# Kernel optimization log

Hardware: AMD Instinct MI355X
Metric: run time of the kernel (lower is better)

## Reference

```python
import jax, jax.numpy as jnp
import numpy as np

N_NODES = 50000
N_EDGES = 800000
D_IN, D_HID, D_OUT = 96, 96, 48


def _gcn_conv(x, src, dst, W, b, num_nodes):
    """PyG GCNConv: h = x @ W; out[dst] += norm * h[src]; out += b.
    Symmetric normalization deg^{-1/2}[src] * deg^{-1/2}[dst], self-loops included
    (src/dst already contain self-loops)."""
    h = x @ W  # [N, d_out]
    deg = jax.ops.segment_sum(jnp.ones_like(dst, dtype=h.dtype), dst,
                              num_segments=num_nodes)  # in-degree incl. self-loop
    dinv = jnp.where(deg > 0, jax.lax.rsqrt(deg), 0.0)
    norm = dinv[src] * dinv[dst]  # [E+N]
    msgs = h[src] * norm[:, None]  # gather + scale (the memory-bound part)
    out = jax.ops.segment_sum(msgs, dst, num_segments=num_nodes)  # scatter-add
    return out + b


def setup_inputs() -> dict:
    key = jax.random.key(0)
    k1, k2, k3, k4 = jax.random.split(key, 4)
    x = jax.random.normal(k1, (N_NODES, D_IN), dtype=jnp.float32)
    edge_index = jax.random.randint(k2, (2, N_EDGES), 0, N_NODES, dtype=jnp.int64)
    # Glorot-ish init for weights, zero bias (matches GCNConv defaults)
    W1 = jax.random.normal(k3, (D_IN, D_HID), dtype=jnp.float32) / np.sqrt(D_IN)
    b1 = jnp.zeros((D_HID,), dtype=jnp.float32)
    W2 = jax.random.normal(k4, (D_HID, D_OUT), dtype=jnp.float32) / np.sqrt(D_HID)
    b2 = jnp.zeros((D_OUT,), dtype=jnp.float32)
    return {"x": x, "edge_index": edge_index, "W1": W1, "b1": b1, "W2": W2, "b2": b2}


def reference(x, edge_index, W1, b1, W2, b2):
    num_nodes = x.shape[0]
    loops = jnp.arange(num_nodes, dtype=edge_index.dtype)
    src = jnp.concatenate([edge_index[0], loops])  # add self-loops
    dst = jnp.concatenate([edge_index[1], loops])
    h = _gcn_conv(x, src, dst, W1, b1, num_nodes)
    h = jax.nn.relu(h)
    # dropout p=0.5 is identity in eval mode (self.training=False)
    out = _gcn_conv(h, src, dst, W2, b2, num_nodes)
    return out
```

## Files before the change

kernel.cpp:

```cpp
#include <hip/hip_runtime.h>
#include <hip/hip_bf16.h>


constexpr int NN = 50000;
constexpr int NE = 800000;
constexpr int DI = 96;
constexpr int DH = 96;
constexpr int DO = 48;

constexpr int BK_SHIFT = 6;
constexpr int NBK      = (NN + 63) >> 6;
constexpr int BK_CAP   = 2048;

constexpr int NCHUNK = 256;
constexpr int CH     = (NE + NCHUNK - 1) / NCHUNK;

constexpr int G1_ROWS = 64;
constexpr int NG1     = (NN + G1_ROWS - 1) / G1_ROWS;

typedef unsigned short us4 __attribute__((ext_vector_type(4)));
typedef unsigned short us8 __attribute__((ext_vector_type(8)));

__device__ __forceinline__ float bf2f(unsigned short u) {
    return __uint_as_float(((unsigned int)u) << 16);
}
__device__ __forceinline__ unsigned short f2bf(float f) {
    __hip_bfloat16 b = __float2bfloat16(f);
    return *reinterpret_cast<unsigned short*>(&b);
}


__global__ __launch_bounds__(256) void k_hist(const int* __restrict__ dst,
                                              int* __restrict__ C, int e) {
    __shared__ int hist[NBK];
    for (int i = threadIdx.x; i < NBK; i += 256) hist[i] = 0;
    __syncthreads();
    const int blk = blockIdx.x;
    const int beg = blk * CH, end = min(beg + CH, e);
    for (int i = beg + threadIdx.x; i < end; i += 256)
        atomicAdd(&hist[dst[i] >> BK_SHIFT], 1);
    __syncthreads();
    for (int b = threadIdx.x; b < NBK; b += 256)
        C[b * NCHUNK + blk] = hist[b];
}

__global__ __launch_bounds__(256) void k_rowscan(int* __restrict__ C,
                                                 int* __restrict__ totals,
                                                 int* __restrict__ row_ptr) {
    if (blockIdx.x == 0 && threadIdx.x == 0) row_ptr[NN] = NE;
    const int w    = threadIdx.x >> 6;
    const int lane = threadIdx.x & 63;
    const int r    = blockIdx.x * 4 + w;
    if (r >= NBK) return;
    int* row = C + r * NCHUNK;
    int v[4], s[4];
#pragma unroll
    for (int q = 0; q < 4; ++q) { v[q] = row[q * 64 + lane]; s[q] = v[q]; }
#pragma unroll
    for (int off = 1; off < 64; off <<= 1) {
#pragma unroll
        for (int q = 0; q < 4; ++q) {
            int y = __shfl_up(s[q], off);
            if (lane >= off) s[q] += y;
        }
    }
    int c0 = __shfl(s[0], 63);
    int c1 = __shfl(s[1], 63);
    int c2 = __shfl(s[2], 63);
    s[1] += c0;
    s[2] += c0 + c1;
    s[3] += c0 + c1 + c2;
#pragma unroll
    for (int q = 0; q < 4; ++q) row[q * 64 + lane] = s[q] - v[q];
    if (lane == 63) totals[r] = s[3];
}

__global__ __launch_bounds__(256) void k_scatter_gemm1(
        const int* __restrict__ src, const int* __restrict__ dst,
        const int* __restrict__ C, const int* __restrict__ totals,
        int* __restrict__ bk_ptr, unsigned* __restrict__ ebuf, int e,
        const float* __restrict__ X, const float* __restrict__ W,
        unsigned short* __restrict__ H, int n) {
    __shared__ int bkL[NBK + 1];
    __shared__ int part[256];
    __shared__ int cur[NBK];
    constexpr int P = 97;
    __shared__ float ws[DI * DH];
    __shared__ float xs[G1_ROWS * P];

    const int t = threadIdx.x;

    if (blockIdx.x < NCHUNK) {
        int v[4];
        int s = 0;
        const int base = t * 4;
#pragma unroll
        for (int i = 0; i < 4; ++i) {
            int idx = base + i;
            v[i] = (idx < NBK) ? totals[idx] : 0;
            s += v[i];
        }
        part[t] = s;
        __syncthreads();
#pragma unroll
        for (int off = 1; off < 256; off <<= 1) {
            int x = part[t];
            int a = (t >= off) ? part[t - off] : 0;
            __syncthreads();
            part[t] = x + a;
            __syncthreads();
        }
        int run = part[t] - s;
#pragma unroll
        for (int i = 0; i < 4; ++i) {
            int idx = base + i;
            if (idx <= NBK) bkL[idx] = run;
            run += v[i];
        }
        __syncthreads();

        const int blk = blockIdx.x;
        for (int b = t; b < NBK; b += 256) cur[b] = bkL[b] + C[b * NCHUNK + blk];
        if (blk == 0)
            for (int i = t; i <= NBK; i += 256) bk_ptr[i] = bkL[i];
        __syncthreads();

        const int beg = blk * CH, end = min(beg + CH, e);
        for (int i = beg + t; i < end; i += 256) {
            int d = dst[i];
            int b = d >> BK_SHIFT;
            int pos = atomicAdd(&cur[b], 1);
            ebuf[pos] = ((unsigned)(d & 63) << 16) | (unsigned)src[i];
        }
    } else {
        const int row0 = (blockIdx.x - NCHUNK) * G1_ROWS;
        unsigned short* hout = reinterpret_cast<unsigned short*>(xs);

        for (int i = t; i < DI * DH; i += 256) ws[i] = W[i];
        {
            const float4* Xv = reinterpret_cast<const float4*>(X + (size_t)row0 * DI);
            const int nv   = G1_ROWS * DI / 4;
            const int maxv = ((n - row0) * DI) / 4;
            for (int i = t; i < nv; i += 256) {
                float4 v = (i < maxv) ? Xv[i] : float4{0.f, 0.f, 0.f, 0.f};
                int r = i / 24, c = (i % 24) * 4;
                xs[r * P + c + 0] = v.x;
                xs[r * P + c + 1] = v.y;
                xs[r * P + c + 2] = v.z;
                xs[r * P + c + 3] = v.w;
            }
        }
        __syncthreads();

        const int cg = t & 15, rg = t >> 4;
        float acc[4][6] = {};
#pragma unroll 2
        for (int k = 0; k < DI; ++k) {
            float xv[4];
#pragma unroll
            for (int i = 0; i < 4; ++i) xv[i] = xs[(rg * 4 + i) * P + k];
#pragma unroll
            for (int j = 0; j < 6; ++j) {
                float wv = ws[k * DH + cg * 6 + j];
#pragma unroll
                for (int i = 0; i < 4; ++i) acc[i][j] += xv[i] * wv;
            }
        }
        __syncthreads();

#pragma unroll
        for (int i = 0; i < 4; ++i) {
#pragma unroll
            for (int j = 0; j < 6; ++j)
                hout[(rg * 4 + i) * 96 + cg * 6 + j] = f2bf(acc[i][j]);
        }
        __syncthreads();

        {
            const us8* ho8 = reinterpret_cast<const us8*>(hout);
            us8* H8 = reinterpret_cast<us8*>(H + (size_t)row0 * DH);
            const int nv   = G1_ROWS * DH / 8;
            const int maxv = ((n - row0) * DH) / 8;
            for (int i = t; i < nv && i < maxv; i += 256) H8[i] = ho8[i];
        }
    }
}

__global__ __launch_bounds__(256) void k_bsort(const unsigned* __restrict__ ebuf,
                                               const int* __restrict__ bk_ptr,
                                               int* __restrict__ row_ptr,
                                               float* __restrict__ dinv,
                                               unsigned short* __restrict__ src16, int n) {
    __shared__ unsigned eL[BK_CAP];
    __shared__ unsigned short outL[BK_CAP];
    __shared__ int curL[64];
    __shared__ int baseL[64];

    const int b   = blockIdx.x;
    const int beg = bk_ptr[b];
    const int m   = bk_ptr[b + 1] - beg;
    const int t   = threadIdx.x;

    if (t < 64) curL[t] = 0;
    __syncthreads();

    for (int i = t; i < m; i += 256) {
        unsigned v = ebuf[beg + i];
        eL[i] = v;
        atomicAdd(&curL[v >> 16], 1);
    }
    __syncthreads();

    if (t < 64) {
        int c = curL[t];
        int x = c;
#pragma unroll
        for (int off = 1; off < 64; off <<= 1) {
            int y = __shfl_up(x, off);
            if (t >= off) x += y;
        }
        int excl = x - c;
        baseL[t] = excl;
        int d0 = (b << BK_SHIFT) + t;
        if (d0 < n) {
            row_ptr[d0] = beg + excl;
            dinv[d0]    = rsqrtf((float)(c + 1));
        }
    }
    __syncthreads();
    if (t < 64) curL[t] = baseL[t];
    __syncthreads();

    for (int i = t; i < m; i += 256) {
        unsigned v = eL[i];
        int p = atomicAdd(&curL[v >> 16], 1);
        outL[p] = (unsigned short)(v & 0xFFFFu);
    }
    __syncthreads();
    for (int i = t; i < m; i += 256) src16[beg + i] = outL[i];
}

__global__ __launch_bounds__(256) void k_pack(const unsigned short* __restrict__ src16,
                                              const float* __restrict__ dinv,
                                              unsigned* __restrict__ epack, int e) {
    int i2 = (blockIdx.x * 256 + threadIdx.x) * 2;
    if (i2 + 1 < e) {
        unsigned pairv = *reinterpret_cast<const unsigned*>(src16 + i2);
        unsigned s0 = pairv & 0xFFFFu;
        unsigned s1 = pairv >> 16;
        unsigned w0 = f2bf(dinv[s0]);
        unsigned w1 = f2bf(dinv[s1]);
        uint2 o;
        o.x = (w0 << 16) | s0;
        o.y = (w1 << 16) | s1;
        *reinterpret_cast<uint2*>(epack + i2) = o;
    } else if (i2 < e) {
        unsigned s0 = src16[i2];
        epack[i2] = ((unsigned)f2bf(dinv[s0]) << 16) | s0;
    }
}


__global__ __launch_bounds__(768) void k_agg1_gemm2(
        const unsigned short* __restrict__ h1,
        const float* __restrict__ dinv,
        const int* __restrict__ row_ptr,
        const unsigned* __restrict__ epack,
        const float* __restrict__ b1,
        const float* __restrict__ W2,
        unsigned short* __restrict__ h2, int n) {
    constexpr int P2 = 104;
    __shared__ unsigned short a1t[G1_ROWS * P2];
    __shared__ float ws[DH * DO];

    const int t = threadIdx.x;
    for (int i = t; i < DH * DO; i += 768) ws[i] = W2[i];

    const int rloc = t / 12;
    const int g    = t % 12;
    const int node = blockIdx.x * G1_ROWS + rloc;

    if (node < n) {
        const us8* h8 = reinterpret_cast<const us8*>(h1);
        const float di = dinv[node];

        float accA[8], accB[8];
        {
            us8 hv = h8[(size_t)node * 12 + g];
#pragma unroll
            for (int j = 0; j < 8; ++j) { accA[j] = di * bf2f(hv[j]); accB[j] = 0.f; }
        }

        const int beg = row_ptr[node];
        const int end = row_ptr[node + 1];
        int k = beg;
        int kA = min((beg + 7) & ~7, end);
        for (; k < kA; ++k) {
            unsigned ev = epack[k];
            float w = bf2f((unsigned short)(ev >> 16));
            us8 vv = h8[(size_t)(ev & 0xFFFFu) * 12 + g];
#pragma unroll
            for (int j = 0; j < 8; ++j) accA[j] += w * bf2f(vv[j]);
        }
        for (; k + 8 <= end; k += 8) {
            const uint4* ev4 = reinterpret_cast<const uint4*>(epack + k);
            uint4 e0 = ev4[0], e1 = ev4[1];
            us8 v0 = h8[(size_t)(e0.x & 0xFFFFu) * 12 + g];
            us8 v1 = h8[(size_t)(e0.y & 0xFFFFu) * 12 + g];
            us8 v2 = h8[(size_t)(e0.z & 0xFFFFu) * 12 + g];
            us8 v3 = h8[(size_t)(e0.w & 0xFFFFu) * 12 + g];
            us8 v4 = h8[(size_t)(e1.x & 0xFFFFu) * 12 + g];
            us8 v5 = h8[(size_t)(e1.y & 0xFFFFu) * 12 + g];
            us8 v6 = h8[(size_t)(e1.z & 0xFFFFu) * 12 + g];
            us8 v7 = h8[(size_t)(e1.w & 0xFFFFu) * 12 + g];
            float w0 = bf2f((unsigned short)(e0.x >> 16));
            float w1 = bf2f((unsigned short)(e0.y >> 16));
            float w2 = bf2f((unsigned short)(e0.z >> 16));
            float w3 = bf2f((unsigned short)(e0.w >> 16));
            float w4 = bf2f((unsigned short)(e1.x >> 16));
            float w5 = bf2f((unsigned short)(e1.y >> 16));
            float w6 = bf2f((unsigned short)(e1.z >> 16));
            float w7 = bf2f((unsigned short)(e1.w >> 16));
#pragma unroll
            for (int j = 0; j < 8; ++j) {
                accA[j] += w0 * bf2f(v0[j]) + w1 * bf2f(v1[j])
                         + w4 * bf2f(v4[j]) + w5 * bf2f(v5[j]);
                accB[j] += w2 * bf2f(v2[j]) + w3 * bf2f(v3[j])
                         + w6 * bf2f(v6[j]) + w7 * bf2f(v7[j]);
            }
        }
        for (; k < end; ++k) {
            unsigned ev = epack[k];
            float w = bf2f((unsigned short)(ev >> 16));
            us8 vv = h8[(size_t)(ev & 0xFFFFu) * 12 + g];
#pragma unroll
            for (int j = 0; j < 8; ++j) accB[j] += w * bf2f(vv[j]);
        }

        us8 o;
#pragma unroll
        for (int j = 0; j < 8; ++j) {
            float r = di * (accA[j] + accB[j]) + b1[g * 8 + j];
            o[j] = f2bf(fmaxf(r, 0.f));
        }
        *reinterpret_cast<us8*>(a1t + rloc * P2 + g * 8) = o;
    }
    __syncthreads();

    const int c0 = g * 4;
    float acc[4] = {};
#pragma unroll 2
    for (int k = 0; k < DH; ++k) {
        float xv = bf2f(a1t[rloc * P2 + k]);
#pragma unroll
        for (int j = 0; j < 4; ++j) acc[j] += xv * ws[k * DO + c0 + j];
    }
    if (node < n) {
        float dv = dinv[node];
        us4 o;
#pragma unroll
        for (int j = 0; j < 4; ++j) o[j] = f2bf(acc[j] * dv);
        *reinterpret_cast<us4*>(h2 + (size_t)node * DO + c0) = o;
    }
}


template<int D, bool RELU>
__global__ __launch_bounds__(256) void k_agg_csr(const unsigned short* __restrict__ h,
                                                 const float* __restrict__ dinv,
                                                 const int* __restrict__ row_ptr,
                                                 const unsigned short* __restrict__ src16,
                                                 const float* __restrict__ bias,
                                                 float* __restrict__ outp, int n) {
    constexpr int G = D / 8;
    int t = blockIdx.x * blockDim.x + threadIdx.x;
    if (t >= n * G) return;
    const int node = t / G;
    const int g    = t % G;

    const us8* h8 = reinterpret_cast<const us8*>(h);

    float accA[8], accB[8];
    {
        us8 hv = h8[(size_t)node * G + g];
#pragma unroll
        for (int j = 0; j < 8; ++j) { accA[j] = bf2f(hv[j]); accB[j] = 0.f; }
    }

    const int beg = row_ptr[node];
    const int end = row_ptr[node + 1];
    int k = beg;
    int kA = min((beg + 7) & ~7, end);
    for (; k < kA; ++k) {
        us8 vv = h8[(size_t)src16[k] * G + g];
#pragma unroll
        for (int j = 0; j < 8; ++j) accA[j] += bf2f(vv[j]);
    }
    for (; k + 8 <= end; k += 8) {
        us8 si = *reinterpret_cast<const us8*>(src16 + k);
        us8 v0 = h8[(size_t)si[0] * G + g];
        us8 v1 = h8[(size_t)si[1] * G + g];
        us8 v2 = h8[(size_t)si[2] * G + g];
        us8 v3 = h8[(size_t)si[3] * G + g];
        us8 v4 = h8[(size_t)si[4] * G + g];
        us8 v5 = h8[(size_t)si[5] * G + g];
        us8 v6 = h8[(size_t)si[6] * G + g];
        us8 v7 = h8[(size_t)si[7] * G + g];
#pragma unroll
        for (int j = 0; j < 8; ++j) {
            accA[j] += (bf2f(v0[j]) + bf2f(v1[j])) + (bf2f(v4[j]) + bf2f(v5[j]));
            accB[j] += (bf2f(v2[j]) + bf2f(v3[j])) + (bf2f(v6[j]) + bf2f(v7[j]));
        }
    }
    for (; k < end; ++k) {
        us8 vv = h8[(size_t)src16[k] * G + g];
#pragma unroll
        for (int j = 0; j < 8; ++j) accB[j] += bf2f(vv[j]);
    }

    const float di = dinv[node];
    const float4* b4 = reinterpret_cast<const float4*>(bias);
    float4 b0 = b4[g * 2], b1 = b4[g * 2 + 1];
    float r[8];
#pragma unroll
    for (int j = 0; j < 8; ++j) r[j] = di * (accA[j] + accB[j]);
    r[0] += b0.x; r[1] += b0.y; r[2] += b0.z; r[3] += b0.w;
    r[4] += b1.x; r[5] += b1.y; r[6] += b1.z; r[7] += b1.w;
    if (RELU) {
#pragma unroll
        for (int j = 0; j < 8; ++j) r[j] = fmaxf(r[j], 0.f);
    }
    float4* o4 = reinterpret_cast<float4*>(outp + (size_t)node * D + g * 8);
    o4[0] = float4{r[0], r[1], r[2], r[3]};
    o4[1] = float4{r[4], r[5], r[6], r[7]};
}


extern "C" void kernel_launch(void* const* d_in, const int* in_sizes, int n_in,
                              void* d_out, int out_size, void* d_ws, size_t ws_size,
                              hipStream_t stream) {
    const float* x   = (const float*)d_in[0];
    const int*   ei  = (const int*)d_in[1];
    const float* W1  = (const float*)d_in[2];
    const float* b1  = (const float*)d_in[3];
    const float* W2  = (const float*)d_in[4];
    const float* b2  = (const float*)d_in[5];
    float*       out = (float*)d_out;

    const int* srcv = ei;
    const int* dstv = ei + NE;

    char* p = (char*)d_ws;
    float*          dinv  = (float*)p;           p += (size_t)NN * 4;
    unsigned short* h1    = (unsigned short*)p;  p += (size_t)NN * DH * 2;
    unsigned short* h2    = (unsigned short*)p;  p += (size_t)NN * DO * 2;
    int*      row_ptr     = (int*)p;             p += (size_t)(NN + 16) * 4;
    unsigned short* src16 = (unsigned short*)p;  p += (size_t)NE * 2;
    unsigned* epack       = (unsigned*)p;        p += (size_t)NE * 4;
    unsigned* ebuf        = (unsigned*)p;        p += (size_t)NE * 4;
    int*      Cm          = (int*)p;             p += (size_t)NBK * NCHUNK * 4;
    int*      totals      = (int*)p;             p += (size_t)NBK * 4;
    int*      bk_ptr      = (int*)p;             p += (size_t)(NBK + 1) * 4;

    const int B = 256;

    k_hist<<<NCHUNK, B, 0, stream>>>(dstv, Cm, NE);
    k_rowscan<<<(NBK + 3) / 4, B, 0, stream>>>(Cm, totals, row_ptr);
    k_scatter_gemm1<<<NCHUNK + NG1, B, 0, stream>>>(
        srcv, dstv, Cm, totals, bk_ptr, ebuf, NE, x, W1, h1, NN);
    k_bsort<<<NBK, B, 0, stream>>>(ebuf, bk_ptr, row_ptr, dinv, src16, NN);
    k_pack<<<(NE / 2 + B - 1) / B, B, 0, stream>>>(src16, dinv, epack, NE);

    k_agg1_gemm2<<<NG1, 768, 0, stream>>>(h1, dinv, row_ptr, epack, b1, W2, h2, NN);

    {
        int total = NN * (DO / 8);
        k_agg_csr<DO, false><<<(total + B - 1) / B, B, 0, stream>>>(
            h2, dinv, row_ptr, src16, b2, out, NN);
    }
}
```

Baseline: 120.8 us.

## Split fused layer-1 aggregation and GEMM2 into separate kernels

```diff
diff --git a/kernel.cpp b/kernel.cpp
--- a/kernel.cpp
+++ b/kernel.cpp
@@ -261,118 +261,153 @@
 }
 
 
-__global__ __launch_bounds__(768) void k_agg1_gemm2(
-        const unsigned short* __restrict__ h1,
-        const float* __restrict__ dinv,
-        const int* __restrict__ row_ptr,
-        const unsigned* __restrict__ epack,
-        const float* __restrict__ b1,
-        const float* __restrict__ W2,
-        unsigned short* __restrict__ h2, int n) {
-    constexpr int P2 = 104;
-    __shared__ unsigned short a1t[G1_ROWS * P2];
+__global__ __launch_bounds__(256) void k_agg1(const unsigned short* __restrict__ h1,
+                                              const float* __restrict__ dinv,
+                                              const int* __restrict__ row_ptr,
+                                              const unsigned* __restrict__ epack,
+                                              const float* __restrict__ b1,
+                                              unsigned short* __restrict__ a1, int n) {
+    constexpr int G = 12;
+    int t = blockIdx.x * blockDim.x + threadIdx.x;
+    if (t >= n * G) return;
+    const int node = t / G;
+    const int g    = t % G;
+
+    const us8* h8 = reinterpret_cast<const us8*>(h1);
+    const float di = dinv[node];
+
+    float accA[8], accB[8];
+    {
+        us8 hv = h8[(size_t)node * G + g];
+#pragma unroll
+        for (int j = 0; j < 8; ++j) { accA[j] = di * bf2f(hv[j]); accB[j] = 0.f; }
+    }
+
+    const int beg = row_ptr[node];
+    const int end = row_ptr[node + 1];
+    int k = beg;
+    int kA = min((beg + 7) & ~7, end);
+    for (; k < kA; ++k) {
+        unsigned ev = epack[k];
+        float w = bf2f((unsigned short)(ev >> 16));
+        us8 vv = h8[(size_t)(ev & 0xFFFFu) * G + g];
+#pragma unroll
+        for (int j = 0; j < 8; ++j) accA[j] += w * bf2f(vv[j]);
+    }
+    for (; k + 8 <= end; k += 8) {
+        const uint4* ev4 = reinterpret_cast<const uint4*>(epack + k);
+        uint4 e0 = ev4[0], e1 = ev4[1];
+        us8 v0 = h8[(size_t)(e0.x & 0xFFFFu) * G + g];
+        us8 v1 = h8[(size_t)(e0.y & 0xFFFFu) * G + g];
+        us8 v2 = h8[(size_t)(e0.z & 0xFFFFu) * G + g];
+        us8 v3 = h8[(size_t)(e0.w & 0xFFFFu) * G + g];
+        us8 v4 = h8[(size_t)(e1.x & 0xFFFFu) * G + g];
+        us8 v5 = h8[(size_t)(e1.y & 0xFFFFu) * G + g];
+        us8 v6 = h8[(size_t)(e1.z & 0xFFFFu) * G + g];
+        us8 v7 = h8[(size_t)(e1.w & 0xFFFFu) * G + g];
+        float w0 = bf2f((unsigned short)(e0.x >> 16));
+        float w1 = bf2f((unsigned short)(e0.y >> 16));
+        float w2 = bf2f((unsigned short)(e0.z >> 16));
+        float w3 = bf2f((unsigned short)(e0.w >> 16));
+        float w4 = bf2f((unsigned short)(e1.x >> 16));
+        float w5 = bf2f((unsigned short)(e1.y >> 16));
+        float w6 = bf2f((unsigned short)(e1.z >> 16));
+        float w7 = bf2f((unsigned short)(e1.w >> 16));
+#pragma unroll
+        for (int j = 0; j < 8; ++j) {
+            accA[j] += w0 * bf2f(v0[j]) + w1 * bf2f(v1[j])
+                     + w4 * bf2f(v4[j]) + w5 * bf2f(v5[j]);
+            accB[j] += w2 * bf2f(v2[j]) + w3 * bf2f(v3[j])
+                     + w6 * bf2f(v6[j]) + w7 * bf2f(v7[j]);
+        }
+    }
+    for (; k < end; ++k) {
+        unsigned ev = epack[k];
+        float w = bf2f((unsigned short)(ev >> 16));
+        us8 vv = h8[(size_t)(ev & 0xFFFFu) * G + g];
+#pragma unroll
+        for (int j = 0; j < 8; ++j) accB[j] += w * bf2f(vv[j]);
+    }
+
+    us8 o;
+#pragma unroll
+    for (int j = 0; j < 8; ++j) {
+        float r = di * (accA[j] + accB[j]) + b1[g * 8 + j];
+        o[j] = f2bf(fmaxf(r, 0.f));
+    }
+    reinterpret_cast<us8*>(a1)[(size_t)node * G + g] = o;
+}
+
+
+__global__ __launch_bounds__(256) void k_gemm2(const unsigned short* __restrict__ A,
+                                               const float* __restrict__ W,
+                                               const float* __restrict__ dinv,
+                                               unsigned short* __restrict__ H, int n) {
+    constexpr int ROWS = 64, P = 98;
     __shared__ float ws[DH * DO];
-
-    const int t = threadIdx.x;
-    for (int i = t; i < DH * DO; i += 768) ws[i] = W2[i];
-
-    const int rloc = t / 12;
-    const int g    = t % 12;
-    const int node = blockIdx.x * G1_ROWS + rloc;
-
-    if (node < n) {
-        const us8* h8 = reinterpret_cast<const us8*>(h1);
-        const float di = dinv[node];
-
-        float accA[8], accB[8];
-        {
-            us8 hv = h8[(size_t)node * 12 + g];
-#pragma unroll
-            for (int j = 0; j < 8; ++j) { accA[j] = di * bf2f(hv[j]); accB[j] = 0.f; }
-        }
-
-        const int beg = row_ptr[node];
-        const int end = row_ptr[node + 1];
-        int k = beg;
-        int kA = min((beg + 7) & ~7, end);
-        for (; k < kA; ++k) {
-            unsigned ev = epack[k];
-            float w = bf2f((unsigned short)(ev >> 16));
-            us8 vv = h8[(size_t)(ev & 0xFFFFu) * 12 + g];
-#pragma unroll
-            for (int j = 0; j < 8; ++j) accA[j] += w * bf2f(vv[j]);
-        }
-        for (; k + 8 <= end; k += 8) {
-            const uint4* ev4 = reinterpret_cast<const uint4*>(epack + k);
-            uint4 e0 = ev4[0], e1 = ev4[1];
-            us8 v0 = h8[(size_t)(e0.x & 0xFFFFu) * 12 + g];
-            us8 v1 = h8[(size_t)(e0.y & 0xFFFFu) * 12 + g];
-            us8 v2 = h8[(size_t)(e0.z & 0xFFFFu) * 12 + g];
-            us8 v3 = h8[(size_t)(e0.w & 0xFFFFu) * 12 + g];
-            us8 v4 = h8[(size_t)(e1.x & 0xFFFFu) * 12 + g];
-            us8 v5 = h8[(size_t)(e1.y & 0xFFFFu) * 12 + g];
-            us8 v6 = h8[(size_t)(e1.z & 0xFFFFu) * 12 + g];
-            us8 v7 = h8[(size_t)(e1.w & 0xFFFFu) * 12 + g];
-            float w0 = bf2f((unsigned short)(e0.x >> 16));
-            float w1 = bf2f((unsigned short)(e0.y >> 16));
-            float w2 = bf2f((unsigned short)(e0.z >> 16));
-            float w3 = bf2f((unsigned short)(e0.w >> 16));
-            float w4 = bf2f((unsigned short)(e1.x >> 16));
-            float w5 = bf2f((unsigned short)(e1.y >> 16));
-            float w6 = bf2f((unsigned short)(e1.z >> 16));
-            float w7 = bf2f((unsigned short)(e1.w >> 16));
-#pragma unroll
-            for (int j = 0; j < 8; ++j) {
-                accA[j] += w0 * bf2f(v0[j]) + w1 * bf2f(v1[j])
-                         + w4 * bf2f(v4[j]) + w5 * bf2f(v5[j]);
-                accB[j] += w2 * bf2f(v2[j]) + w3 * bf2f(v3[j])
-                         + w6 * bf2f(v6[j]) + w7 * bf2f(v7[j]);
-            }
-        }
-        for (; k < end; ++k) {
-            unsigned ev = epack[k];
-            float w = bf2f((unsigned short)(ev >> 16));
-            us8 vv = h8[(size_t)(ev & 0xFFFFu) * 12 + g];
-#pragma unroll
-            for (int j = 0; j < 8; ++j) accB[j] += w * bf2f(vv[j]);
-        }
-
-        us8 o;
-#pragma unroll
-        for (int j = 0; j < 8; ++j) {
-            float r = di * (accA[j] + accB[j]) + b1[g * 8 + j];
-            o[j] = f2bf(fmaxf(r, 0.f));
-        }
-        *reinterpret_cast<us8*>(a1t + rloc * P2 + g * 8) = o;
-    }
-    __syncthreads();
-
-    const int c0 = g * 4;
-    float acc[4] = {};
+    __shared__ unsigned short xs[ROWS * P];
+
+    const int tid  = threadIdx.x;
+    const int row0 = blockIdx.x * ROWS;
+
+    for (int i = tid; i < DH * DO; i += 256) ws[i] = W[i];
+    {
+        const us8* Av = reinterpret_cast<const us8*>(A + (size_t)row0 * DH);
+        const int nv   = ROWS * DH / 8;
+        const int maxv = ((n - row0) * DH) / 8;
+        for (int i = tid; i < nv; i += 256) {
+            us8 v = (i < maxv) ? Av[i] : (us8)(0);
+            int r = i / 12, c = (i % 12) * 8;
+#pragma unroll
+            for (int jj = 0; jj < 8; ++jj) xs[r * P + c + jj] = v[jj];
+        }
+    }
+    __syncthreads();
+
+    const int cg = tid & 15, rg = tid >> 4;
+    float acc[4][3] = {};
 #pragma unroll 2
     for (int k = 0; k < DH; ++k) {
-        float xv = bf2f(a1t[rloc * P2 + k]);
-#pragma unroll
-        for (int j = 0; j < 4; ++j) acc[j] += xv * ws[k * DO + c0 + j];
-    }
-    if (node < n) {
-        float dv = dinv[node];
-        us4 o;
-#pragma unroll
-        for (int j = 0; j < 4; ++j) o[j] = f2bf(acc[j] * dv);
-        *reinterpret_cast<us4*>(h2 + (size_t)node * DO + c0) = o;
-    }
-}
-
-
-template<int D, bool RELU>
-__global__ __launch_bounds__(256) void k_agg_csr(const unsigned short* __restrict__ h,
-                                                 const float* __restrict__ dinv,
-                                                 const int* __restrict__ row_ptr,
-                                                 const unsigned short* __restrict__ src16,
-                                                 const float* __restrict__ bias,
-                                                 float* __restrict__ outp, int n) {
-    constexpr int G = D / 8;
+        float xv[4];
+#pragma unroll
+        for (int i = 0; i < 4; ++i) xv[i] = bf2f(xs[(rg * 4 + i) * P + k]);
+#pragma unroll
+        for (int j = 0; j < 3; ++j) {
+            float wv = ws[k * DO + cg * 3 + j];
+#pragma unroll
+            for (int i = 0; i < 4; ++i) acc[i][j] += xv[i] * wv;
+        }
+    }
+    __syncthreads();
+
+    unsigned short* hout = xs;
+#pragma unroll
+    for (int i = 0; i < 4; ++i) {
+        int row = row0 + rg * 4 + i;
+        float dv = (row < n) ? dinv[row] : 0.f;
+#pragma unroll
+        for (int j = 0; j < 3; ++j)
+            hout[(rg * 4 + i) * 48 + cg * 3 + j] = f2bf(acc[i][j] * dv);
+    }
+    __syncthreads();
+
+    {
+        const us8* ho8 = reinterpret_cast<const us8*>(hout);
+        us8* H8 = reinterpret_cast<us8*>(H + (size_t)row0 * DO);
+        const int nv   = ROWS * DO / 8;
+        const int maxv = ((n - row0) * DO) / 8;
+        for (int i = tid; i < nv && i < maxv; i += 256) H8[i] = ho8[i];
+    }
+}
+
+
+__global__ __launch_bounds__(256) void k_agg2(const unsigned short* __restrict__ h,
+                                              const float* __restrict__ dinv,
+                                              const int* __restrict__ row_ptr,
+                                              const unsigned short* __restrict__ src16,
+                                              const float* __restrict__ bias,
+                                              float* __restrict__ outp, int n) {
+    constexpr int G = 6;
     int t = blockIdx.x * blockDim.x + threadIdx.x;
     if (t >= n * G) return;
     const int node = t / G;
@@ -426,11 +461,7 @@
     for (int j = 0; j < 8; ++j) r[j] = di * (accA[j] + accB[j]);
     r[0] += b0.x; r[1] += b0.y; r[2] += b0.z; r[3] += b0.w;
     r[4] += b1.x; r[5] += b1.y; r[6] += b1.z; r[7] += b1.w;
-    if (RELU) {
-#pragma unroll
-        for (int j = 0; j < 8; ++j) r[j] = fmaxf(r[j], 0.f);
-    }
-    float4* o4 = reinterpret_cast<float4*>(outp + (size_t)node * D + g * 8);
+    float4* o4 = reinterpret_cast<float4*>(outp + (size_t)node * DO + g * 8);
     o4[0] = float4{r[0], r[1], r[2], r[3]};
     o4[1] = float4{r[4], r[5], r[6], r[7]};
 }
@@ -453,6 +484,7 @@
     char* p = (char*)d_ws;
     float*          dinv  = (float*)p;           p += (size_t)NN * 4;
     unsigned short* h1    = (unsigned short*)p;  p += (size_t)NN * DH * 2;
+    unsigned short* a1    = (unsigned short*)p;  p += (size_t)NN * DH * 2;
     unsigned short* h2    = (unsigned short*)p;  p += (size_t)NN * DO * 2;
     int*      row_ptr     = (int*)p;             p += (size_t)(NN + 16) * 4;
     unsigned short* src16 = (unsigned short*)p;  p += (size_t)NE * 2;
@@ -471,11 +503,15 @@
     k_bsort<<<NBK, B, 0, stream>>>(ebuf, bk_ptr, row_ptr, dinv, src16, NN);
     k_pack<<<(NE / 2 + B - 1) / B, B, 0, stream>>>(src16, dinv, epack, NE);
 
-    k_agg1_gemm2<<<NG1, 768, 0, stream>>>(h1, dinv, row_ptr, epack, b1, W2, h2, NN);
-
     {
-        int total = NN * (DO / 8);
-        k_agg_csr<DO, false><<<(total + B - 1) / B, B, 0, stream>>>(
+        int total = NN * 12;
+        k_agg1<<<(total + B - 1) / B, B, 0, stream>>>(
+            h1, dinv, row_ptr, epack, b1, a1, NN);
+    }
+    k_gemm2<<<(NN + 63) / 64, B, 0, stream>>>(a1, W2, dinv, h2, NN);
+    {
+        int total = NN * 6;
+        k_agg2<<<(total + B - 1) / B, B, 0, stream>>>(
             h2, dinv, row_ptr, src16, b2, out, NN);
     }
 }
```

After: 125.3 us. 3.7% more time.

## Shrink GEMM1 row tile, alias shared memory, and resize agg1 blocks for occupancy

Applied to the files above, without the earlier changes.

```diff
diff --git a/kernel.cpp b/kernel.cpp
--- a/kernel.cpp
+++ b/kernel.cpp
@@ -15,8 +15,11 @@
 constexpr int NCHUNK = 256;
 constexpr int CH     = (NE + NCHUNK - 1) / NCHUNK;
 
-constexpr int G1_ROWS = 64;
+constexpr int G1_ROWS = 32;
 constexpr int NG1     = (NN + G1_ROWS - 1) / G1_ROWS;
+
+constexpr int A2_NODES = 42;
+constexpr int NB2      = (NN + A2_NODES - 1) / A2_NODES;
 
 typedef unsigned short us4 __attribute__((ext_vector_type(4)));
 typedef unsigned short us8 __attribute__((ext_vector_type(8)));
@@ -81,16 +84,16 @@
         int* __restrict__ bk_ptr, unsigned* __restrict__ ebuf, int e,
         const float* __restrict__ X, const float* __restrict__ W,
         unsigned short* __restrict__ H, int n) {
-    __shared__ int bkL[NBK + 1];
-    __shared__ int part[256];
-    __shared__ int cur[NBK];
     constexpr int P = 97;
-    __shared__ float ws[DI * DH];
-    __shared__ float xs[G1_ROWS * P];
+    __shared__ __align__(16) char smem[(DI * DH + G1_ROWS * P) * 4];
 
     const int t = threadIdx.x;
 
     if (blockIdx.x < NCHUNK) {
+        int* bkL  = reinterpret_cast<int*>(smem);
+        int* part = bkL + (NBK + 1);
+        int* cur  = part + 256;
+
         int v[4];
         int s = 0;
         const int base = t * 4;
@@ -133,8 +136,11 @@
             ebuf[pos] = ((unsigned)(d & 63) << 16) | (unsigned)src[i];
         }
     } else {
+        float* ws = reinterpret_cast<float*>(smem);
+        float* xs = ws + DI * DH;
+        unsigned short* hout = reinterpret_cast<unsigned short*>(xs);
+
         const int row0 = (blockIdx.x - NCHUNK) * G1_ROWS;
-        unsigned short* hout = reinterpret_cast<unsigned short*>(xs);
 
         for (int i = t; i < DI * DH; i += 256) ws[i] = W[i];
         {
@@ -153,26 +159,26 @@
         __syncthreads();
 
         const int cg = t & 15, rg = t >> 4;
-        float acc[4][6] = {};
+        float acc[2][6] = {};
 #pragma unroll 2
         for (int k = 0; k < DI; ++k) {
-            float xv[4];
-#pragma unroll
-            for (int i = 0; i < 4; ++i) xv[i] = xs[(rg * 4 + i) * P + k];
+            float xv[2];
+#pragma unroll
+            for (int i = 0; i < 2; ++i) xv[i] = xs[(rg * 2 + i) * P + k];
 #pragma unroll
             for (int j = 0; j < 6; ++j) {
                 float wv = ws[k * DH + cg * 6 + j];
 #pragma unroll
-                for (int i = 0; i < 4; ++i) acc[i][j] += xv[i] * wv;
+                for (int i = 0; i < 2; ++i) acc[i][j] += xv[i] * wv;
             }
         }
         __syncthreads();
 
 #pragma unroll
-        for (int i = 0; i < 4; ++i) {
+        for (int i = 0; i < 2; ++i) {
 #pragma unroll
             for (int j = 0; j < 6; ++j)
-                hout[(rg * 4 + i) * 96 + cg * 6 + j] = f2bf(acc[i][j]);
+                hout[(rg * 2 + i) * 96 + cg * 6 + j] = f2bf(acc[i][j]);
         }
         __syncthreads();
 
@@ -261,7 +267,7 @@
 }
 
 
-__global__ __launch_bounds__(768) void k_agg1_gemm2(
+__global__ __launch_bounds__(512) void k_agg1_gemm2(
         const unsigned short* __restrict__ h1,
         const float* __restrict__ dinv,
         const int* __restrict__ row_ptr,
@@ -270,17 +276,18 @@
         const float* __restrict__ W2,
         unsigned short* __restrict__ h2, int n) {
     constexpr int P2 = 104;
-    __shared__ unsigned short a1t[G1_ROWS * P2];
+    __shared__ unsigned short a1t[A2_NODES * P2];
     __shared__ float ws[DH * DO];
 
     const int t = threadIdx.x;
-    for (int i = t; i < DH * DO; i += 768) ws[i] = W2[i];
+    for (int i = t; i < DH * DO; i += 512) ws[i] = W2[i];
 
     const int rloc = t / 12;
     const int g    = t % 12;
-    const int node = blockIdx.x * G1_ROWS + rloc;
-
-    if (node < n) {
+    const bool active = (t < A2_NODES * 12);
+    const int node = blockIdx.x * A2_NODES + rloc;
+
+    if (active && node < n) {
         const us8* h8 = reinterpret_cast<const us8*>(h1);
         const float di = dinv[node];
 
@@ -347,32 +354,33 @@
     }
     __syncthreads();
 
-    const int c0 = g * 4;
-    float acc[4] = {};
+    if (active) {
+        const int c0 = g * 4;
+        float acc[4] = {};
 #pragma unroll 2
-    for (int k = 0; k < DH; ++k) {
-        float xv = bf2f(a1t[rloc * P2 + k]);
-#pragma unroll
-        for (int j = 0; j < 4; ++j) acc[j] += xv * ws[k * DO + c0 + j];
-    }
-    if (node < n) {
-        float dv = dinv[node];
-        us4 o;
-#pragma unroll
-        for (int j = 0; j < 4; ++j) o[j] = f2bf(acc[j] * dv);
-        *reinterpret_cast<us4*>(h2 + (size_t)node * DO + c0) = o;
-    }
-}
-
-
-template<int D, bool RELU>
-__global__ __launch_bounds__(256) void k_agg_csr(const unsigned short* __restrict__ h,
-                                                 const float* __restrict__ dinv,
-                                                 const int* __restrict__ row_ptr,
-                                                 const unsigned short* __restrict__ src16,
-                                                 const float* __restrict__ bias,
-                                                 float* __restrict__ outp, int n) {
-    constexpr int G = D / 8;
+        for (int k = 0; k < DH; ++k) {
+            float xv = bf2f(a1t[rloc * P2 + k]);
+#pragma unroll
+            for (int j = 0; j < 4; ++j) acc[j] += xv * ws[k * DO + c0 + j];
+        }
+        if (node < n) {
+            float dv = dinv[node];
+            us4 o;
+#pragma unroll
+            for (int j = 0; j < 4; ++j) o[j] = f2bf(acc[j] * dv);
+            *reinterpret_cast<us4*>(h2 + (size_t)node * DO + c0) = o;
+        }
+    }
+}
+
+
+__global__ __launch_bounds__(256) void k_agg2(const unsigned short* __restrict__ h,
+                                              const float* __restrict__ dinv,
+                                              const int* __restrict__ row_ptr,
+                                              const unsigned short* __restrict__ src16,
+                                              const float* __restrict__ bias,
+                                              float* __restrict__ outp, int n) {
+    constexpr int G = 6;
     int t = blockIdx.x * blockDim.x + threadIdx.x;
     if (t >= n * G) return;
     const int node = t / G;
@@ -426,11 +434,7 @@
     for (int j = 0; j < 8; ++j) r[j] = di * (accA[j] + accB[j]);
     r[0] += b0.x; r[1] += b0.y; r[2] += b0.z; r[3] += b0.w;
     r[4] += b1.x; r[5] += b1.y; r[6] += b1.z; r[7] += b1.w;
-    if (RELU) {
-#pragma unroll
-        for (int j = 0; j < 8; ++j) r[j] = fmaxf(r[j], 0.f);
-    }
-    float4* o4 = reinterpret_cast<float4*>(outp + (size_t)node * D + g * 8);
+    float4* o4 = reinterpret_cast<float4*>(outp + (size_t)node * DO + g * 8);
     o4[0] = float4{r[0], r[1], r[2], r[3]};
     o4[1] = float4{r[4], r[5], r[6], r[7]};
 }
@@ -471,11 +475,11 @@
     k_bsort<<<NBK, B, 0, stream>>>(ebuf, bk_ptr, row_ptr, dinv, src16, NN);
     k_pack<<<(NE / 2 + B - 1) / B, B, 0, stream>>>(src16, dinv, epack, NE);
 
-    k_agg1_gemm2<<<NG1, 768, 0, stream>>>(h1, dinv, row_ptr, epack, b1, W2, h2, NN);
+    k_agg1_gemm2<<<NB2, 512, 0, stream>>>(h1, dinv, row_ptr, epack, b1, W2, h2, NN);
 
     {
-        int total = NN * (DO / 8);
-        k_agg_csr<DO, false><<<(total + B - 1) / B, B, 0, stream>>>(
+        int total = NN * 6;
+        k_agg2<<<(total + B - 1) / B, B, 0, stream>>>(
             h2, dinv, row_ptr, src16, b2, out, NN);
     }
 }
```

New measurement: 116.4 us (median of 2 runs). 3.6% less time.
